# Performance work log

Measured on AMD Instinct MI355X. Metric: run time of the kernel, lower is better.

## Reference

```python
import jax, jax.numpy as jnp
import numpy as np

EMBED_DIM = 512
NUM_HEADS = 8
HEAD_DIM = EMBED_DIM // NUM_HEADS


def setup_inputs() -> dict:
    key = jax.random.key(0)
    ks = jax.random.split(key, 9)
    C = EMBED_DIM
    s = 1.0 / np.sqrt(C)
    x = jax.random.normal(ks[0], (1, 4096, C), dtype=jnp.float32)
    Wq = jax.random.uniform(ks[1], (C, C), jnp.float32, -s, s)
    bq = jax.random.uniform(ks[2], (C,), jnp.float32, -s, s)
    Wk = jax.random.uniform(ks[3], (C, C), jnp.float32, -s, s)
    bk = jax.random.uniform(ks[4], (C,), jnp.float32, -s, s)
    Wv = jax.random.uniform(ks[5], (C, C), jnp.float32, -s, s)
    bv = jax.random.uniform(ks[6], (C,), jnp.float32, -s, s)
    Wo = jax.random.uniform(ks[7], (C, C), jnp.float32, -s, s)
    bo = jax.random.uniform(ks[8], (C,), jnp.float32, -s, s)
    return {"x": x, "Wq": Wq, "bq": bq, "Wk": Wk, "bk": bk,
            "Wv": Wv, "bv": bv, "Wo": Wo, "bo": bo}


def reference(x, Wq, bq, Wk, bk, Wv, bv, Wo, bo):
    B, N, C = x.shape
    H, D = NUM_HEADS, HEAD_DIM
    # QKV projections, split into heads: [B, H, N, D]
    def proj(W, b):
        y = x @ W + b
        return y.reshape(B, N, H, D).transpose(0, 2, 1, 3)
    Q, K, V = proj(Wq, bq), proj(Wk, bk), proj(Wv, bv)
    # NOTE: original scales by 1/sqrt(embed_dim), NOT 1/sqrt(head_dim)
    scale = 1.0 / jnp.sqrt(jnp.float32(C)).astype(x.dtype)
    scores = jnp.einsum('bhnd,bhmd->bhnm', Q, K) * scale  # [B,H,N,N]
    attn = jax.nn.softmax(scores, axis=-1)
    out = jnp.einsum('bhnm,bhmd->bhnd', attn, V)  # [B,H,N,D]
    out = out.transpose(0, 2, 1, 3).reshape(B, N, C)
    return out @ Wo + bo
```

## Files before the change

### kernel.cpp

```cpp
#include <hip/hip_runtime.h>
#include <hip/hip_bf16.h>

#define SEQ 4096
#define CDIM 512
#define NHEAD 8
#define HDIM 64
#define KVB 64
#define NSPLIT 2
#define TILES_PER_SPLIT (SEQ / KVB / NSPLIT)

typedef __attribute__((ext_vector_type(8))) short bf16x8;
typedef __attribute__((ext_vector_type(4))) float f32x4;
typedef __attribute__((ext_vector_type(16))) float f32x16;

__device__ __forceinline__ short f2b(float f) {
  union { float f; unsigned u; } v; v.f = f;
  unsigned u = v.u;
  unsigned r = u + 0x7fffu + ((u >> 16) & 1u);
  return (short)(r >> 16);
}
__device__ __forceinline__ float b2f(short s) {
  union { unsigned u; float f; } v; v.u = ((unsigned)(unsigned short)s) << 16;
  return v.f;
}
__device__ __forceinline__ unsigned pk2(float a, float b) {
  union { __hip_bfloat162 h; unsigned u; } z;
  z.h = __float22bfloat162_rn(make_float2(a, b));
  return z.u;
}

__global__ __launch_bounds__(256) void prep_kernel(
    const float* __restrict__ x,
    const float* __restrict__ Wq, const float* __restrict__ Wk,
    const float* __restrict__ Wv, const float* __restrict__ Wo,
    short* __restrict__ xb,
    short* __restrict__ Wqt, short* __restrict__ Wkt,
    short* __restrict__ Wvt, short* __restrict__ Wot) {
  __shared__ short tile[32][33];
  int b = blockIdx.x, tid = threadIdx.x;
  if (b < 2048) {
    int i = (b * 256 + tid) * 4;
    float4 v = *(const float4*)(x + i);
    short4 o;
    o.x = f2b(v.x); o.y = f2b(v.y); o.z = f2b(v.z); o.w = f2b(v.w);
    *(short4*)(xb + i) = o;
    return;
  }
  int t = b - 2048;
  int mat = t >> 8; t &= 255;
  const float* W = mat == 0 ? Wq : mat == 1 ? Wk : mat == 2 ? Wv : Wo;
  short* Wt = mat == 0 ? Wqt : mat == 1 ? Wkt : mat == 2 ? Wvt : Wot;
  int n0 = (t & 15) * 32, k0 = (t >> 4) * 32;
  int tx = tid & 31, ty = tid >> 5;
  for (int i = 0; i < 32; i += 8)
    tile[ty + i][tx] = f2b(W[(size_t)(k0 + ty + i) * CDIM + n0 + tx]);
  __syncthreads();
  for (int i = 0; i < 32; i += 8)
    Wt[(size_t)(n0 + ty + i) * CDIM + k0 + tx] = tile[tx][ty + i];
}

__global__ __launch_bounds__(256) void qkv64_kernel(
    const short* __restrict__ A,
    const short* __restrict__ Wqt, const short* __restrict__ Wkt, const short* __restrict__ Wvt,
    const float* __restrict__ bq, const float* __restrict__ bk, const float* __restrict__ bv,
    short* __restrict__ Qb, short* __restrict__ Kb, short* __restrict__ Vtb) {
  __shared__ __align__(16) short As[64 * 64];
  __shared__ __align__(16) short Bs[64 * 64];
  const int z = blockIdx.z;
  const short* Bt = z == 0 ? Wqt : z == 1 ? Wkt : Wvt;
  const float* bias = z == 0 ? bq : z == 1 ? bk : bv;
  const int m0 = blockIdx.x * 64, n0 = blockIdx.y * 64;
  f32x16 acc = {};
  const int tid = threadIdx.x;
  const int wid = tid >> 6, lane = tid & 63, l31 = lane & 31, hi = lane >> 5;
  const int wr = wid >> 1, wc = wid & 1;
  for (int kt = 0; kt < CDIM; kt += 64) {
    __syncthreads();
#pragma unroll
    for (int i = 0; i < 2; ++i) {
      int idx = i * 256 + tid, row = idx >> 3, seg = idx & 7;
      int sc = (seg ^ (row & 7)) * 8;
      __builtin_amdgcn_global_load_lds(
          (const __attribute__((address_space(1))) void*)(A + (size_t)(m0 + row) * CDIM + kt + sc),
          (__attribute__((address_space(3))) void*)(As + idx * 8), 16, 0, 0);
    }
#pragma unroll
    for (int i = 0; i < 2; ++i) {
      int idx = i * 256 + tid, row = idx >> 3, seg = idx & 7;
      int sc = (seg ^ (row & 7)) * 8;
      __builtin_amdgcn_global_load_lds(
          (const __attribute__((address_space(1))) void*)(Bt + (size_t)(n0 + row) * CDIM + kt + sc),
          (__attribute__((address_space(3))) void*)(Bs + idx * 8), 16, 0, 0);
    }
    __syncthreads();
#pragma unroll
    for (int ks = 0; ks < 4; ++ks) {
      int brow = wc * 32 + l31;
      bf16x8 bfr = *(const bf16x8*)(Bs + brow * 64 + ((ks * 16 + hi * 8) ^ ((brow & 7) * 8)));
      int arow = wr * 32 + l31;
      bf16x8 afr = *(const bf16x8*)(As + arow * 64 + ((ks * 16 + hi * 8) ^ ((arow & 7) * 8)));
      acc = __builtin_amdgcn_mfma_f32_32x32x16_bf16(afr, bfr, acc, 0, 0, 0);
    }
  }
  const int ncol = n0 + wc * 32 + l31;
  const float bn = bias[ncol];
  if (z != 2) {
    short* D = z == 0 ? Qb : Kb;
#pragma unroll
    for (int r = 0; r < 16; ++r) {
      int m = m0 + wr * 32 + (r & 3) + 8 * (r >> 2) + 4 * hi;
      D[(size_t)m * CDIM + ncol] = f2b(acc[r] + bn);
    }
  } else {
#pragma unroll
    for (int r = 0; r < 16; ++r) {
      int m = m0 + wr * 32 + (r & 3) + 8 * (r >> 2) + 4 * hi;
      Vtb[(size_t)ncol * SEQ + m] = f2b(acc[r] + bn);
    }
  }
}

__global__ __launch_bounds__(256) void out64_kernel(
    const short* __restrict__ A, const short* __restrict__ Bt,
    const float* __restrict__ bias, float* __restrict__ out) {
  __shared__ __align__(16) short As[64 * 64];
  __shared__ __align__(16) short Bs[64 * 64];
  const int m0 = blockIdx.x * 64, n0 = blockIdx.y * 64;
  f32x16 acc = {};
  const int tid = threadIdx.x;
  const int wid = tid >> 6, lane = tid & 63, l31 = lane & 31, hi = lane >> 5;
  const int wr = wid >> 1, wc = wid & 1;
  for (int kt = 0; kt < CDIM; kt += 64) {
    __syncthreads();
#pragma unroll
    for (int i = 0; i < 2; ++i) {
      int idx = i * 256 + tid, row = idx >> 3, seg = idx & 7;
      int sc = (seg ^ (row & 7)) * 8;
      __builtin_amdgcn_global_load_lds(
          (const __attribute__((address_space(1))) void*)(A + (size_t)(m0 + row) * CDIM + kt + sc),
          (__attribute__((address_space(3))) void*)(As + idx * 8), 16, 0, 0);
    }
#pragma unroll
    for (int i = 0; i < 2; ++i) {
      int idx = i * 256 + tid, row = idx >> 3, seg = idx & 7;
      int sc = (seg ^ (row & 7)) * 8;
      __builtin_amdgcn_global_load_lds(
          (const __attribute__((address_space(1))) void*)(Bt + (size_t)(n0 + row) * CDIM + kt + sc),
          (__attribute__((address_space(3))) void*)(Bs + idx * 8), 16, 0, 0);
    }
    __syncthreads();
#pragma unroll
    for (int ks = 0; ks < 4; ++ks) {
      int brow = wc * 32 + l31;
      bf16x8 bfr = *(const bf16x8*)(Bs + brow * 64 + ((ks * 16 + hi * 8) ^ ((brow & 7) * 8)));
      int arow = wr * 32 + l31;
      bf16x8 afr = *(const bf16x8*)(As + arow * 64 + ((ks * 16 + hi * 8) ^ ((arow & 7) * 8)));
      acc = __builtin_amdgcn_mfma_f32_32x32x16_bf16(afr, bfr, acc, 0, 0, 0);
    }
  }
  const int ncol = n0 + wc * 32 + l31;
  const float bn = bias[ncol];
#pragma unroll
  for (int r = 0; r < 16; ++r) {
    int m = m0 + wr * 32 + (r & 3) + 8 * (r >> 2) + 4 * hi;
    out[(size_t)m * CDIM + ncol] = acc[r] + bn;
  }
}

__global__ __launch_bounds__(256) void combine_kernel(
    const short* __restrict__ p0, const short* __restrict__ p1,
    const float* __restrict__ lpart, short* __restrict__ Ab) {
  int t = blockIdx.x * 256 + threadIdx.x;
  size_t base = (size_t)t * 8;
  int q = (int)(base >> 9), c = (int)(base & 511), h = c >> 6;
  float l = lpart[(size_t)h * SEQ + q] + lpart[(size_t)(NHEAD + h) * SEQ + q];
  float rinv = 1.f / l;
  bf16x8 a0 = *(const bf16x8*)(p0 + base);
  bf16x8 a1 = *(const bf16x8*)(p1 + base);
  short ov[8];
#pragma unroll
  for (int i = 0; i < 8; ++i)
    ov[i] = f2b((b2f(a0[i]) + b2f(a1[i])) * rinv);
  *(bf16x8*)(Ab + base) = *(bf16x8*)(ov);
}

__global__ __launch_bounds__(512, 4) void attn_kernel(
    const short* __restrict__ Qb,
    const short* __restrict__ Kb,
    const short* __restrict__ Vtb,
    short* __restrict__ Op0, short* __restrict__ Op1,
    float* __restrict__ lpart) {
  __shared__ __align__(16) char arena[49152];
  __shared__ float lzp[4][32];
  short* KsB = (short*)arena;
  short* VsB = (short*)(arena + 24576);
  const int bid = blockIdx.x;
  const int h = bid & 7;
  const int rest = bid >> 3;
  const int split = rest & 1;
  const int q0 = (rest >> 1) * 128;
  const int kvbase = split * (TILES_PER_SPLIT * KVB);
  const int tid = threadIdx.x;
  const int wid = tid >> 6, lane = tid & 63;
  const int l31 = lane & 31, hi = lane >> 5;
  const int rh = wid >> 1, kq = wid & 1;
  const float scale2 = 0.06375872274f;

  short* Opart = split == 0 ? Op0 : Op1;

  bf16x8 qf[4];
  {
    int qrow = q0 + rh * 32 + l31;
#pragma unroll
    for (int kst = 0; kst < 4; ++kst) {
      bf16x8 q = *(const bf16x8*)(Qb + (size_t)qrow * CDIM + h * 64 + kst * 16 + hi * 8);
#pragma unroll
      for (int i = 0; i < 8; ++i) q[i] = f2b(b2f(q[i]) * scale2);
      qf[kst] = q;
    }
  }

  const int srow = tid >> 3;
  const int scol8 = 8 * ((tid & 7) ^ (srow & 7));
  const short* kstage = Kb + (size_t)(kvbase + srow) * CDIM + h * 64 + scol8;
  const short* vstage = Vtb + (size_t)(h * 64 + srow) * SEQ + kvbase + scol8;
  auto stage = [&](short* sK, short* sV) {
    __builtin_amdgcn_global_load_lds(
        (const __attribute__((address_space(1))) void*)kstage,
        (__attribute__((address_space(3))) void*)(sK + tid * 8), 16, 0, 0);
    __builtin_amdgcn_global_load_lds(
        (const __attribute__((address_space(1))) void*)vstage,
        (__attribute__((address_space(3))) void*)(sV + tid * 8), 16, 0, 0);
    kstage += KVB * CDIM;
    vstage += KVB;
  };

  f32x16 osum[2] = {};
  float lsum = 0.f;
  unsigned w[8];

  auto softmax = [&](f32x16& s) {
    float ls0 = 0.f, ls1 = 0.f;
#pragma unroll
    for (int m = 0; m < 8; ++m) {
      float p0 = __builtin_amdgcn_exp2f(s[2 * m]);
      float p1 = __builtin_amdgcn_exp2f(s[2 * m + 1]);
      ls0 += p0; ls1 += p1;
      w[m] = pk2(p0, p1);
    }
    lsum += ls0 + ls1;
  };

  auto mk_pf = [&](unsigned* u0, unsigned* u1) {
#if __has_builtin(__builtin_amdgcn_permlane32_swap)
    auto a0 = __builtin_amdgcn_permlane32_swap(w[0], w[2], false, false);
    auto a1 = __builtin_amdgcn_permlane32_swap(w[1], w[3], false, false);
    auto a2 = __builtin_amdgcn_permlane32_swap(w[4], w[6], false, false);
    auto a3 = __builtin_amdgcn_permlane32_swap(w[5], w[7], false, false);
    u0[0] = a0[0]; u0[1] = a1[0]; u0[2] = a0[1]; u0[3] = a1[1];
    u1[0] = a2[0]; u1[1] = a3[0]; u1[2] = a2[1]; u1[3] = a3[1];
#else
    unsigned t0 = hi ? w[0] : w[2], t1 = hi ? w[1] : w[3];
    unsigned t2 = hi ? w[4] : w[6], t3 = hi ? w[5] : w[7];
    unsigned r0 = __shfl_xor(t0, 32), r1 = __shfl_xor(t1, 32);
    unsigned r2 = __shfl_xor(t2, 32), r3 = __shfl_xor(t3, 32);
    u0[0] = hi ? r0 : w[0]; u0[1] = hi ? r1 : w[1];
    u0[2] = hi ? w[2] : r0; u0[3] = hi ? w[3] : r1;
    u1[0] = hi ? r2 : w[4]; u1[1] = hi ? r3 : w[5];
    u1[2] = hi ? w[6] : r2; u1[3] = hi ? w[7] : r3;
#endif
  };

  auto phase = [&](const short* vbuf, const short* kbuf, short* sK, short* sV, bool do_st) {
    if (do_st) stage(sK, sV);
    union { unsigned u[4]; bf16x8 v; } pf0, pf1;
    mk_pf(pf0.u, pf1.u);
    f32x16 s = {};
    __builtin_amdgcn_s_setprio(1);
#pragma unroll
    for (int kst = 0; kst < 4; ++kst) {
      int row = kq * 32 + l31;
      bf16x8 kf = *(const bf16x8*)(kbuf + row * 64 + ((kst * 16 + hi * 8) ^ ((row & 7) * 8)));
      s = __builtin_amdgcn_mfma_f32_32x32x16_bf16(kf, qf[kst], s, 0, 0, 0);
    }
#pragma unroll
    for (int dm = 0; dm < 2; ++dm) {
      int vrow = dm * 32 + l31;
      bf16x8 vf0 = *(const bf16x8*)(vbuf + vrow * 64 + ((kq * 32 + hi * 8) ^ ((vrow & 7) * 8)));
      osum[dm] = __builtin_amdgcn_mfma_f32_32x32x16_bf16(vf0, pf0.v, osum[dm], 0, 0, 0);
      bf16x8 vf1 = *(const bf16x8*)(vbuf + vrow * 64 + ((kq * 32 + 16 + hi * 8) ^ ((vrow & 7) * 8)));
      osum[dm] = __builtin_amdgcn_mfma_f32_32x32x16_bf16(vf1, pf1.v, osum[dm], 0, 0, 0);
    }
    __builtin_amdgcn_s_setprio(0);
    softmax(s);
    __syncthreads();
  };

  stage(KsB, VsB);
  __syncthreads();
  stage(KsB + 4096, VsB + 4096);
  {
    f32x16 s = {};
#pragma unroll
    for (int kst = 0; kst < 4; ++kst) {
      int row = kq * 32 + l31;
      bf16x8 kf = *(const bf16x8*)(KsB + row * 64 + ((kst * 16 + hi * 8) ^ ((row & 7) * 8)));
      s = __builtin_amdgcn_mfma_f32_32x32x16_bf16(kf, qf[kst], s, 0, 0, 0);
    }
    softmax(s);
  }
  __syncthreads();

  for (int t = 0; t + 3 < TILES_PER_SPLIT; t += 3) {
    phase(VsB,        KsB + 4096, KsB + 8192, VsB + 8192, true);
    phase(VsB + 4096, KsB + 8192, KsB,        VsB,        true);
    phase(VsB + 8192, KsB,        KsB + 4096, VsB + 4096, true);
  }
  phase(VsB, KsB + 4096, KsB, VsB, false);

  {
    union { unsigned u[4]; bf16x8 v; } pf0, pf1;
    mk_pf(pf0.u, pf1.u);
    const short* vb = VsB + 4096;
#pragma unroll
    for (int dm = 0; dm < 2; ++dm) {
      int vrow = dm * 32 + l31;
      bf16x8 vf0 = *(const bf16x8*)(vb + vrow * 64 + ((kq * 32 + hi * 8) ^ ((vrow & 7) * 8)));
      osum[dm] = __builtin_amdgcn_mfma_f32_32x32x16_bf16(vf0, pf0.v, osum[dm], 0, 0, 0);
      bf16x8 vf1 = *(const bf16x8*)(vb + vrow * 64 + ((kq * 32 + 16 + hi * 8) ^ ((vrow & 7) * 8)));
      osum[dm] = __builtin_amdgcn_mfma_f32_32x32x16_bf16(vf1, pf1.v, osum[dm], 0, 0, 0);
    }
  }

  lsum += __shfl_xor(lsum, 32);

  __syncthreads();
  float* bufA = (float*)arena;
#define OD(dm, r) ((dm) * 32 + ((r) & 3) + 8 * ((r) >> 2) + 4 * hi)
#define OADDR(dm, r) (rh * 2112 + OD(dm, r) * 33 + l31)
  if (kq == 1) {
    if (hi == 0) lzp[rh][l31] = lsum;
#pragma unroll
    for (int dm = 0; dm < 2; ++dm)
#pragma unroll
      for (int r = 0; r < 16; ++r) bufA[OADDR(dm, r)] = osum[dm][r];
  }
  __syncthreads();
  if (kq == 0) {
#pragma unroll
    for (int dm = 0; dm < 2; ++dm)
#pragma unroll
      for (int r = 0; r < 16; ++r) {
        float v = osum[dm][r] + bufA[OADDR(dm, r)];
        bufA[OADDR(dm, r)] = v;
      }
    float lt = lsum + lzp[rh][l31];
    if (hi == 0)
      lpart[(size_t)(split * NHEAD + h) * SEQ + q0 + rh * 32 + l31] = lt;
  }
  __syncthreads();
#undef OD
#undef OADDR

  {
    int q_ = tid >> 2;
    int dc = (tid & 3) * 16;
    int qr = q_ >> 5, ql = q_ & 31;
    short ov[16];
#pragma unroll
    for (int i = 0; i < 16; ++i)
      ov[i] = f2b(bufA[qr * 2112 + (dc + i) * 33 + ql]);
    *(bf16x8*)(Opart + (size_t)(q0 + q_) * CDIM + h * 64 + dc) = *(bf16x8*)(ov);
    *(bf16x8*)(Opart + (size_t)(q0 + q_) * CDIM + h * 64 + dc + 8) = *(bf16x8*)(ov + 8);
  }
}

extern "C" void kernel_launch(void* const* d_in, const int* in_sizes, int n_in,
                              void* d_out, int out_size, void* d_ws, size_t ws_size,
                              hipStream_t stream) {
  const float* x  = (const float*)d_in[0];
  const float* Wq = (const float*)d_in[1];
  const float* bq = (const float*)d_in[2];
  const float* Wk = (const float*)d_in[3];
  const float* bk = (const float*)d_in[4];
  const float* Wv = (const float*)d_in[5];
  const float* bv = (const float*)d_in[6];
  const float* Wo = (const float*)d_in[7];
  const float* bo = (const float*)d_in[8];
  float* out = (float*)d_out;

  short* ws = (short*)d_ws;
  size_t off = 0;
  short* xb  = ws + off; off += (size_t)SEQ * CDIM;
  short* Wqt = ws + off; off += (size_t)CDIM * CDIM;
  short* Wkt = ws + off; off += (size_t)CDIM * CDIM;
  short* Wvt = ws + off; off += (size_t)CDIM * CDIM;
  short* Wot = ws + off; off += (size_t)CDIM * CDIM;
  short* Qb  = ws + off; off += (size_t)SEQ * CDIM;
  short* Kb  = ws + off; off += (size_t)SEQ * CDIM;
  short* Vtb = ws + off; off += (size_t)CDIM * SEQ;
  short* Ab  = ws + off; off += (size_t)SEQ * CDIM;
  short* Op1 = ws + off; off += (size_t)SEQ * CDIM;
  float* lpart = (float*)(ws + off); off += (size_t)NSPLIT * NHEAD * SEQ * 2;
  short* Op0 = xb;

  prep_kernel<<<2048 + 4 * 256, 256, 0, stream>>>(x, Wq, Wk, Wv, Wo, xb, Wqt, Wkt, Wvt, Wot);
  qkv64_kernel<<<dim3(SEQ / 64, CDIM / 64, 3), 256, 0, stream>>>(
      xb, Wqt, Wkt, Wvt, bq, bk, bv, Qb, Kb, Vtb);
  attn_kernel<<<(SEQ / 128) * NHEAD * NSPLIT, 512, 0, stream>>>(
      Qb, Kb, Vtb, Op0, Op1, lpart);
  combine_kernel<<<SEQ * CDIM / 8 / 256, 256, 0, stream>>>(Op0, Op1, lpart, Ab);
  out64_kernel<<<dim3(SEQ / 64, CDIM / 64), 256, 0, stream>>>(Ab, Wot, bo, out);
}
```

Measured before the change: 77.67 us.

## Deepen K/V LDS pipeline to four buffers with partial vmcnt waits

Grows the LDS arena from three to four K/V tile buffers and prefetches three tiles before the main loop. Full __syncthreads is replaced with s_waitcnt vmcnt(N) plus s_barrier, so a wave waits only for the oldest outstanding tile load rather than draining every load. This is meant to hide global-to-LDS latency behind the MFMA and softmax work. The larger LDS footprint (64KB+) may cut how many blocks fit per CU, against the launch bounds of 4, and the hand-counted vmcnt values depend on how many loads stage issues.

```diff
diff --git a/kernel.cpp b/kernel.cpp
--- a/kernel.cpp
+++ b/kernel.cpp
@@ -190,10 +190,10 @@
     const short* __restrict__ Vtb,
     short* __restrict__ Op0, short* __restrict__ Op1,
     float* __restrict__ lpart) {
-  __shared__ __align__(16) char arena[49152];
+  __shared__ __align__(16) char arena[65536];
   __shared__ float lzp[4][32];
   short* KsB = (short*)arena;
-  short* VsB = (short*)(arena + 24576);
+  short* VsB = (short*)(arena + 32768);
   const int bid = blockIdx.x;
   const int h = bid & 7;
   const int rest = bid >> 3;
@@ -271,7 +271,8 @@
 #endif
   };
 
-  auto phase = [&](const short* vbuf, const short* kbuf, short* sK, short* sV, bool do_st) {
+  auto phase = [&](const short* vbuf, const short* kbuf, short* sK, short* sV,
+                   bool do_st, bool drain) {
     if (do_st) stage(sK, sV);
     union { unsigned u[4]; bf16x8 v; } pf0, pf1;
     mk_pf(pf0.u, pf1.u);
@@ -293,12 +294,18 @@
     }
     __builtin_amdgcn_s_setprio(0);
     softmax(s);
-    __syncthreads();
+    if (drain) asm volatile("s_waitcnt vmcnt(0)" ::: "memory");
+    else       asm volatile("s_waitcnt vmcnt(2)" ::: "memory");
+    __builtin_amdgcn_s_barrier();
+    __builtin_amdgcn_sched_barrier(0);
   };
 
   stage(KsB, VsB);
-  __syncthreads();
   stage(KsB + 4096, VsB + 4096);
+  stage(KsB + 8192, VsB + 8192);
+  asm volatile("s_waitcnt vmcnt(4)" ::: "memory");
+  __builtin_amdgcn_s_barrier();
+  __builtin_amdgcn_sched_barrier(0);
   {
     f32x16 s = {};
 #pragma unroll
@@ -309,19 +316,24 @@
     }
     softmax(s);
   }
-  __syncthreads();
-
-  for (int t = 0; t + 3 < TILES_PER_SPLIT; t += 3) {
-    phase(VsB,        KsB + 4096, KsB + 8192, VsB + 8192, true);
-    phase(VsB + 4096, KsB + 8192, KsB,        VsB,        true);
-    phase(VsB + 8192, KsB,        KsB + 4096, VsB + 4096, true);
-  }
-  phase(VsB, KsB + 4096, KsB, VsB, false);
+  asm volatile("s_waitcnt vmcnt(2)" ::: "memory");
+  __builtin_amdgcn_s_barrier();
+  __builtin_amdgcn_sched_barrier(0);
+
+  for (int t = 0; t < 28; t += 4) {
+    phase(VsB,           KsB + 4096,  KsB + 12288, VsB + 12288, true, false);
+    phase(VsB + 4096,    KsB + 8192,  KsB,         VsB,         true, false);
+    phase(VsB + 8192,    KsB + 12288, KsB + 4096,  VsB + 4096,  true, false);
+    phase(VsB + 12288,   KsB,         KsB + 8192,  VsB + 8192,  true, false);
+  }
+  phase(VsB,        KsB + 4096,  KsB + 12288, VsB + 12288, true,  false);
+  phase(VsB + 4096, KsB + 8192,  nullptr,     nullptr,     false, true);
+  phase(VsB + 8192, KsB + 12288, nullptr,     nullptr,     false, true);
 
   {
     union { unsigned u[4]; bf16x8 v; } pf0, pf1;
     mk_pf(pf0.u, pf1.u);
-    const short* vb = VsB + 4096;
+    const short* vb = VsB + 12288;
 #pragma unroll
     for (int dm = 0; dm < 2; ++dm) {
       int vrow = dm * 32 + l31;
```

Result: slower. 117.1 us (+50.8%).

## Use 128-wide KV tiles with simple double buffering instead of software-pipelined triple buffer

Applied to the files above, without the earlier changes.

Doubles the KV tile to 128 keys per stage and replaces the three-buffer software pipeline, where QK^T for one tile overlapped PV for the previous tile, with a plain double buffer. Each phase now computes QK^T, softmax and PV for the same tile in sequence. The aim is to halve the number of barriers and loop iterations and give each wave more MFMA work per sync. In exchange it raises LDS use to 64KB per block, which may lower occupancy, and it removes the overlap of the exp/softmax step with MFMA.

```diff
diff --git a/kernel.cpp b/kernel.cpp
--- a/kernel.cpp
+++ b/kernel.cpp
@@ -5,9 +5,9 @@
 #define CDIM 512
 #define NHEAD 8
 #define HDIM 64
-#define KVB 64
+#define KVB 128
 #define NSPLIT 2
-#define TILES_PER_SPLIT (SEQ / KVB / NSPLIT)
+#define NT128 (SEQ / KVB / NSPLIT)
 
 typedef __attribute__((ext_vector_type(8))) short bf16x8;
 typedef __attribute__((ext_vector_type(4))) float f32x4;
@@ -190,16 +190,16 @@
     const short* __restrict__ Vtb,
     short* __restrict__ Op0, short* __restrict__ Op1,
     float* __restrict__ lpart) {
-  __shared__ __align__(16) char arena[49152];
+  __shared__ __align__(16) char arena[65536];
   __shared__ float lzp[4][32];
   short* KsB = (short*)arena;
-  short* VsB = (short*)(arena + 24576);
+  short* VsB = (short*)(arena + 32768);
   const int bid = blockIdx.x;
   const int h = bid & 7;
   const int rest = bid >> 3;
   const int split = rest & 1;
   const int q0 = (rest >> 1) * 128;
-  const int kvbase = split * (TILES_PER_SPLIT * KVB);
+  const int kvbase = split * (NT128 * KVB);
   const int tid = threadIdx.x;
   const int wid = tid >> 6, lane = tid & 63;
   const int l31 = lane & 31, hi = lane >> 5;
@@ -220,116 +220,109 @@
     }
   }
 
-  const int srow = tid >> 3;
-  const int scol8 = 8 * ((tid & 7) ^ (srow & 7));
-  const short* kstage = Kb + (size_t)(kvbase + srow) * CDIM + h * 64 + scol8;
-  const short* vstage = Vtb + (size_t)(h * 64 + srow) * SEQ + kvbase + scol8;
+  const int krow = tid >> 3;
+  const int kcol = 8 * ((tid & 7) ^ (krow & 7));
+  const int vrow = tid >> 4;
+  const int vcol = 8 * ((tid & 15) ^ (vrow & 7));
+  const short* kstage = Kb + (size_t)(kvbase + krow) * CDIM + h * 64 + kcol;
+  const short* vstage = Vtb + (size_t)(h * 64 + vrow) * SEQ + kvbase + vcol;
   auto stage = [&](short* sK, short* sV) {
     __builtin_amdgcn_global_load_lds(
         (const __attribute__((address_space(1))) void*)kstage,
         (__attribute__((address_space(3))) void*)(sK + tid * 8), 16, 0, 0);
     __builtin_amdgcn_global_load_lds(
+        (const __attribute__((address_space(1))) void*)(kstage + (size_t)64 * CDIM),
+        (__attribute__((address_space(3))) void*)(sK + tid * 8 + 4096), 16, 0, 0);
+    __builtin_amdgcn_global_load_lds(
         (const __attribute__((address_space(1))) void*)vstage,
         (__attribute__((address_space(3))) void*)(sV + tid * 8), 16, 0, 0);
-    kstage += KVB * CDIM;
+    __builtin_amdgcn_global_load_lds(
+        (const __attribute__((address_space(1))) void*)(vstage + (size_t)32 * SEQ),
+        (__attribute__((address_space(3))) void*)(sV + tid * 8 + 4096), 16, 0, 0);
+    kstage += (size_t)KVB * CDIM;
     vstage += KVB;
   };
 
   f32x16 osum[2] = {};
   float lsum = 0.f;
-  unsigned w[8];
-
-  auto softmax = [&](f32x16& s) {
-    float ls0 = 0.f, ls1 = 0.f;
-#pragma unroll
-    for (int m = 0; m < 8; ++m) {
-      float p0 = __builtin_amdgcn_exp2f(s[2 * m]);
-      float p1 = __builtin_amdgcn_exp2f(s[2 * m + 1]);
-      ls0 += p0; ls1 += p1;
-      w[m] = pk2(p0, p1);
-    }
-    lsum += ls0 + ls1;
-  };
-
-  auto mk_pf = [&](unsigned* u0, unsigned* u1) {
+
+  auto mk_pf = [&](const unsigned* ww, unsigned* u0, unsigned* u1) {
 #if __has_builtin(__builtin_amdgcn_permlane32_swap)
-    auto a0 = __builtin_amdgcn_permlane32_swap(w[0], w[2], false, false);
-    auto a1 = __builtin_amdgcn_permlane32_swap(w[1], w[3], false, false);
-    auto a2 = __builtin_amdgcn_permlane32_swap(w[4], w[6], false, false);
-    auto a3 = __builtin_amdgcn_permlane32_swap(w[5], w[7], false, false);
+    auto a0 = __builtin_amdgcn_permlane32_swap(ww[0], ww[2], false, false);
+    auto a1 = __builtin_amdgcn_permlane32_swap(ww[1], ww[3], false, false);
+    auto a2 = __builtin_amdgcn_permlane32_swap(ww[4], ww[6], false, false);
+    auto a3 = __builtin_amdgcn_permlane32_swap(ww[5], ww[7], false, false);
     u0[0] = a0[0]; u0[1] = a1[0]; u0[2] = a0[1]; u0[3] = a1[1];
     u1[0] = a2[0]; u1[1] = a3[0]; u1[2] = a2[1]; u1[3] = a3[1];
 #else
-    unsigned t0 = hi ? w[0] : w[2], t1 = hi ? w[1] : w[3];
-    unsigned t2 = hi ? w[4] : w[6], t3 = hi ? w[5] : w[7];
+    unsigned t0 = hi ? ww[0] : ww[2], t1 = hi ? ww[1] : ww[3];
+    unsigned t2 = hi ? ww[4] : ww[6], t3 = hi ? ww[5] : ww[7];
     unsigned r0 = __shfl_xor(t0, 32), r1 = __shfl_xor(t1, 32);
     unsigned r2 = __shfl_xor(t2, 32), r3 = __shfl_xor(t3, 32);
-    u0[0] = hi ? r0 : w[0]; u0[1] = hi ? r1 : w[1];
-    u0[2] = hi ? w[2] : r0; u0[3] = hi ? w[3] : r1;
-    u1[0] = hi ? r2 : w[4]; u1[1] = hi ? r3 : w[5];
-    u1[2] = hi ? w[6] : r2; u1[3] = hi ? w[7] : r3;
+    u0[0] = hi ? r0 : ww[0]; u0[1] = hi ? r1 : ww[1];
+    u0[2] = hi ? ww[2] : r0; u0[3] = hi ? ww[3] : r1;
+    u1[0] = hi ? r2 : ww[4]; u1[1] = hi ? r3 : ww[5];
+    u1[2] = hi ? ww[6] : r2; u1[3] = hi ? ww[7] : r3;
 #endif
   };
 
-  auto phase = [&](const short* vbuf, const short* kbuf, short* sK, short* sV, bool do_st) {
+  auto phase = [&](const short* kb, const short* vb, short* sK, short* sV, bool do_st) {
     if (do_st) stage(sK, sV);
-    union { unsigned u[4]; bf16x8 v; } pf0, pf1;
-    mk_pf(pf0.u, pf1.u);
-    f32x16 s = {};
+    f32x16 s0 = {}, s1 = {};
     __builtin_amdgcn_s_setprio(1);
 #pragma unroll
     for (int kst = 0; kst < 4; ++kst) {
-      int row = kq * 32 + l31;
-      bf16x8 kf = *(const bf16x8*)(kbuf + row * 64 + ((kst * 16 + hi * 8) ^ ((row & 7) * 8)));
-      s = __builtin_amdgcn_mfma_f32_32x32x16_bf16(kf, qf[kst], s, 0, 0, 0);
-    }
-#pragma unroll
-    for (int dm = 0; dm < 2; ++dm) {
-      int vrow = dm * 32 + l31;
-      bf16x8 vf0 = *(const bf16x8*)(vbuf + vrow * 64 + ((kq * 32 + hi * 8) ^ ((vrow & 7) * 8)));
-      osum[dm] = __builtin_amdgcn_mfma_f32_32x32x16_bf16(vf0, pf0.v, osum[dm], 0, 0, 0);
-      bf16x8 vf1 = *(const bf16x8*)(vbuf + vrow * 64 + ((kq * 32 + 16 + hi * 8) ^ ((vrow & 7) * 8)));
-      osum[dm] = __builtin_amdgcn_mfma_f32_32x32x16_bf16(vf1, pf1.v, osum[dm], 0, 0, 0);
+      int r0 = kq * 64 + l31;
+      bf16x8 kf0 = *(const bf16x8*)(kb + r0 * 64 + ((kst * 16 + hi * 8) ^ ((r0 & 7) * 8)));
+      s0 = __builtin_amdgcn_mfma_f32_32x32x16_bf16(kf0, qf[kst], s0, 0, 0, 0);
+      int r1 = kq * 64 + 32 + l31;
+      bf16x8 kf1 = *(const bf16x8*)(kb + r1 * 64 + ((kst * 16 + hi * 8) ^ ((r1 & 7) * 8)));
+      s1 = __builtin_amdgcn_mfma_f32_32x32x16_bf16(kf1, qf[kst], s1, 0, 0, 0);
     }
     __builtin_amdgcn_s_setprio(0);
-    softmax(s);
+    unsigned w[16];
+    {
+      float ls = 0.f;
+#pragma unroll
+      for (int m = 0; m < 8; ++m) {
+        float p0 = __builtin_amdgcn_exp2f(s0[2 * m]);
+        float p1 = __builtin_amdgcn_exp2f(s0[2 * m + 1]);
+        ls += p0 + p1;
+        w[m] = pk2(p0, p1);
+      }
+#pragma unroll
+      for (int m = 0; m < 8; ++m) {
+        float p0 = __builtin_amdgcn_exp2f(s1[2 * m]);
+        float p1 = __builtin_amdgcn_exp2f(s1[2 * m + 1]);
+        ls += p0 + p1;
+        w[8 + m] = pk2(p0, p1);
+      }
+      lsum += ls;
+    }
+#pragma unroll
+    for (int half = 0; half < 2; ++half) {
+      union { unsigned u[4]; bf16x8 v; } pf0, pf1;
+      mk_pf(w + half * 8, pf0.u, pf1.u);
+      __builtin_amdgcn_s_setprio(1);
+#pragma unroll
+      for (int dm = 0; dm < 2; ++dm) {
+        int vr = dm * 32 + l31;
+        int cA = kq * 64 + half * 32 + hi * 8;
+        bf16x8 vf0 = *(const bf16x8*)(vb + vr * 128 + (cA ^ ((vr & 7) * 8)));
+        osum[dm] = __builtin_amdgcn_mfma_f32_32x32x16_bf16(vf0, pf0.v, osum[dm], 0, 0, 0);
+        bf16x8 vf1 = *(const bf16x8*)(vb + vr * 128 + ((cA + 16) ^ ((vr & 7) * 8)));
+        osum[dm] = __builtin_amdgcn_mfma_f32_32x32x16_bf16(vf1, pf1.v, osum[dm], 0, 0, 0);
+      }
+      __builtin_amdgcn_s_setprio(0);
+    }
     __syncthreads();
   };
 
   stage(KsB, VsB);
   __syncthreads();
-  stage(KsB + 4096, VsB + 4096);
-  {
-    f32x16 s = {};
-#pragma unroll
-    for (int kst = 0; kst < 4; ++kst) {
-      int row = kq * 32 + l31;
-      bf16x8 kf = *(const bf16x8*)(KsB + row * 64 + ((kst * 16 + hi * 8) ^ ((row & 7) * 8)));
-      s = __builtin_amdgcn_mfma_f32_32x32x16_bf16(kf, qf[kst], s, 0, 0, 0);
-    }
-    softmax(s);
-  }
-  __syncthreads();
-
-  for (int t = 0; t + 3 < TILES_PER_SPLIT; t += 3) {
-    phase(VsB,        KsB + 4096, KsB + 8192, VsB + 8192, true);
-    phase(VsB + 4096, KsB + 8192, KsB,        VsB,        true);
-    phase(VsB + 8192, KsB,        KsB + 4096, VsB + 4096, true);
-  }
-  phase(VsB, KsB + 4096, KsB, VsB, false);
-
-  {
-    union { unsigned u[4]; bf16x8 v; } pf0, pf1;
-    mk_pf(pf0.u, pf1.u);
-    const short* vb = VsB + 4096;
-#pragma unroll
-    for (int dm = 0; dm < 2; ++dm) {
-      int vrow = dm * 32 + l31;
-      bf16x8 vf0 = *(const bf16x8*)(vb + vrow * 64 + ((kq * 32 + hi * 8) ^ ((vrow & 7) * 8)));
-      osum[dm] = __builtin_amdgcn_mfma_f32_32x32x16_bf16(vf0, pf0.v, osum[dm], 0, 0, 0);
-      bf16x8 vf1 = *(const bf16x8*)(vb + vrow * 64 + ((kq * 32 + 16 + hi * 8) ^ ((vrow & 7) * 8)));
-      osum[dm] = __builtin_amdgcn_mfma_f32_32x32x16_bf16(vf1, pf1.v, osum[dm], 0, 0, 0);
-    }
+  for (int t = 0; t < NT128; t += 2) {
+    phase(KsB, VsB, KsB + 8192, VsB + 8192, t + 1 < NT128);
+    phase(KsB + 8192, VsB + 8192, KsB, VsB, t + 2 < NT128);
   }
 
   lsum += __shfl_xor(lsum, 32);
```

Result: no change. 78.80 us (+1.5%).
